# Kernel optimization log

Hardware: AMD Instinct MI355X
Metric: run time of the kernel (lower is better)

The kernel has to match this reference:

```python
import jax, jax.numpy as jnp
import numpy as np

NUM_USERS = 100000
NUM_ITEMS = 50000
EMB_DIM = 64
N_LAYERS = 3
NUM_BICLIQUES = 20000
E_ADJ = 1200000
E_HV = 400000
E_HU = 400000


def setup_inputs() -> dict:
    key = jax.random.key(0)
    ks = jax.random.split(key, 11)
    N = NUM_USERS + NUM_ITEMS
    return {
        "user_emb": jax.random.normal(ks[0], (NUM_USERS, EMB_DIM), dtype=jnp.float32) * 0.1,
        "item_emb": jax.random.normal(ks[1], (NUM_ITEMS, EMB_DIM), dtype=jnp.float32) * 0.1,
        "adj_val": jax.random.uniform(ks[2], (E_ADJ,), dtype=jnp.float32),
        "hv_val": jax.random.uniform(ks[3], (E_HV,), dtype=jnp.float32),
        "hu_val": jax.random.uniform(ks[4], (E_HU,), dtype=jnp.float32),
        "adj_row": jax.random.randint(ks[5], (E_ADJ,), 0, N, dtype=jnp.int32),
        "adj_col": jax.random.randint(ks[6], (E_ADJ,), 0, N, dtype=jnp.int32),
        "hv_row": jax.random.randint(ks[7], (E_HV,), 0, NUM_BICLIQUES, dtype=jnp.int32),
        "hv_col": jax.random.randint(ks[8], (E_HV,), 0, NUM_ITEMS, dtype=jnp.int32),
        "hu_row": jax.random.randint(ks[9], (E_HU,), 0, NUM_USERS, dtype=jnp.int32),
        "hu_col": jax.random.randint(ks[10], (E_HU,), 0, NUM_BICLIQUES, dtype=jnp.int32),
    }


def _spmm(row, col, val, x, n_rows):
    # sparse [n_rows, n_cols] @ dense [n_cols, d] via gather + segment-sum
    return jax.ops.segment_sum(val[:, None] * x[col], row, num_segments=n_rows)


def _row_degree(row, val, n_rows):
    deg = jax.ops.segment_sum(val, row, num_segments=n_rows)
    return jnp.where(deg == 0, 1.0, deg)  # matches degree[degree == 0] = 1.0


def reference(user_emb, item_emb, adj_val, hv_val, hu_val,
              adj_row, adj_col, hv_row, hv_col, hu_row, hu_col):
    N = user_emb.shape[0] + item_emb.shape[0]
    # ---- LightGCN global encoder: mean over layer embeddings ----
    all_emb = jnp.concatenate([user_emb, item_emb], axis=0)  # [N, d]
    acc = all_emb
    e = all_emb
    for _ in range(N_LAYERS):
        e = _spmm(adj_row, adj_col, adj_val, e, N)
        acc = acc + e
    final = acc / (N_LAYERS + 1)
    u_global = final[: user_emb.shape[0]]
    i_global = final[user_emb.shape[0]:]
    # ---- Biclique local encoder ----
    biclique_feat = _spmm(hv_row, hv_col, hv_val, item_emb, NUM_BICLIQUES)  # [B, d]
    biclique_feat = biclique_feat / _row_degree(hv_row, hv_val, NUM_BICLIQUES)[:, None]
    u_local = _spmm(hu_row, hu_col, hu_val, biclique_feat, user_emb.shape[0])  # [U, d]
    u_local = u_local / _row_degree(hu_row, hu_val, user_emb.shape[0])[:, None]
    return (u_global + u_local, i_global)
```

## Files before the change

kernel.cpp:

```cpp
#include <hip/hip_runtime.h>

#define NUSERS 100000
#define NITEMS 50000
#define NTOT   150000
#define NBIC   20000
#define DIM    64

#define HV_BASE  NTOT
#define HU_BASE  (NTOT + NBIC)
#define NROWS_ALL (NTOT + NBIC + NUSERS)

#define ADJ_RPB  500
#define NB_ADJ   300
#define HV_RPB   200
#define NB_HV    100
#define HU_RPB   1000
#define NB_HU    100
#define NBKT     (NB_ADJ + NB_HV + NB_HU)
#define HSIZE    512

#define EDGE_CAP 5120
#define ROWS_CAP 1024
#define CHUNK    8192
#define PA_BLK   1024
#define PB_BLK   512

typedef _Float16 h8 __attribute__((ext_vector_type(8)));

__device__ __forceinline__ void bucket_of(int r, int& b, int& rl) {
    if (r < NTOT)          { int q = r / ADJ_RPB;               b = q;                rl = r - q * ADJ_RPB; }
    else if (r < HU_BASE)  { int rr = r - HV_BASE; int q = rr / HV_RPB;
                             b = NB_ADJ + q;                    rl = rr - q * HV_RPB; }
    else                   { int rr = r - HU_BASE; int q = rr / HU_RPB;
                             b = NB_ADJ + NB_HV + q;            rl = rr - q * HU_RPB; }
}

__global__ void __launch_bounds__(PA_BLK)
phaseA_kernel(const int* __restrict__ adj_row, const int* __restrict__ adj_col,
              const float* __restrict__ adj_val,
              const int* __restrict__ hv_row, const int* __restrict__ hv_col,
              const float* __restrict__ hv_val,
              const int* __restrict__ hu_row, const int* __restrict__ hu_col,
              const float* __restrict__ hu_val,
              const float* __restrict__ user, const float* __restrict__ item,
              _Float16* __restrict__ x16,
              int* __restrict__ bkt_cnt, int2* __restrict__ tmp,
              int e_adj, int e_hv, int e_hu) {
    __shared__ int hist[HSIZE];
    __shared__ int lstart[HSIZE];
    __shared__ int destB[HSIZE];
    __shared__ int psum[HSIZE];
    __shared__ int2 stage[CHUNK];

    const int tid = threadIdx.x;
    const int e_all = e_adj + e_hv + e_hu;
    const int base = blockIdx.x * CHUNK;
    const int nloc = min(CHUNK, e_all - base);

    if (tid < HSIZE) hist[tid] = 0;
    __syncthreads();

    for (int i = tid; i < nloc; i += PA_BLK) {
        int t = base + i, r;
        if (t < e_adj)             r = adj_row[t];
        else if (t < e_adj + e_hv) r = HV_BASE + hv_row[t - e_adj];
        else                       r = HU_BASE + hu_row[t - e_adj - e_hv];
        int b, rl; bucket_of(r, b, rl);
        atomicAdd(&hist[b], 1);
    }
    __syncthreads();

    int v = 0;
    if (tid < HSIZE) { v = hist[tid]; psum[tid] = v; }
    __syncthreads();
    for (int off = 1; off < HSIZE; off <<= 1) {
        int t = 0;
        if (tid < HSIZE && tid >= off) t = psum[tid - off];
        __syncthreads();
        if (tid < HSIZE) psum[tid] += t;
        __syncthreads();
    }
    if (tid < HSIZE) lstart[tid] = psum[tid] - v;
    __syncthreads();

    if (tid < NBKT) {
        int c = hist[tid];
        if (c > 0)
            destB[tid] = tid * EDGE_CAP + atomicAdd(&bkt_cnt[tid], c) - lstart[tid];
    }
    __syncthreads();
    if (tid < HSIZE) hist[tid] = lstart[tid];
    __syncthreads();

    for (int i = tid; i < nloc; i += PA_BLK) {
        int t = base + i, r, c; float v2;
        if (t < e_adj)             { r = adj_row[t]; c = adj_col[t]; v2 = adj_val[t]; }
        else if (t < e_adj + e_hv) { int k = t - e_adj;
                                     r = HV_BASE + hv_row[k]; c = hv_col[k]; v2 = hv_val[k]; }
        else                       { int k = t - e_adj - e_hv;
                                     r = HU_BASE + hu_row[k]; c = hu_col[k]; v2 = hu_val[k]; }
        int b, rl; bucket_of(r, b, rl);
        int p = atomicAdd(&hist[b], 1);
        stage[p] = make_int2(c | (rl << 18), __float_as_int(v2));
    }
    __syncthreads();

    const int wave = tid >> 6, lane = tid & 63;
    for (int b = wave; b < NBKT; b += (PA_BLK / 64)) {
        int s = lstart[b];
        int e = hist[b];
        int d = destB[b];
        for (int j = s + lane; j < e; j += 64)
            tmp[d + j] = stage[j];
    }

    const int n8 = NTOT * DIM / 8;
    const int u8 = NUSERS * DIM / 8;
    const int gsz = gridDim.x * PA_BLK;
    for (int i = blockIdx.x * PA_BLK + tid; i < n8; i += gsz) {
        const float4* src = (i < u8) ? (const float4*)user + 2 * (size_t)i
                                     : (const float4*)item + 2 * (size_t)(i - u8);
        float4 a = src[0], b = src[1];
        h8 h;
        h[0] = (_Float16)a.x; h[1] = (_Float16)a.y; h[2] = (_Float16)a.z; h[3] = (_Float16)a.w;
        h[4] = (_Float16)b.x; h[5] = (_Float16)b.y; h[6] = (_Float16)b.z; h[7] = (_Float16)b.w;
        ((h8*)x16)[i] = h;
    }
}

__global__ void __launch_bounds__(PB_BLK)
phaseB_kernel(const int* __restrict__ bkt_cnt,
              const int2* __restrict__ tmp, int2* __restrict__ edges,
              int* __restrict__ start, int* __restrict__ cntArr) {
    __shared__ int  rh[ROWS_CAP];
    __shared__ int  rs[ROWS_CAP];
    __shared__ int  psum[PB_BLK];
    __shared__ int2 stage[EDGE_CAP];

    const int tid = threadIdx.x;
    const int b = blockIdx.x;
    int rlo, nR;
    if (b < NB_ADJ)              { rlo = b * ADJ_RPB;                          nR = ADJ_RPB; }
    else if (b < NB_ADJ + NB_HV) { rlo = HV_BASE + (b - NB_ADJ) * HV_RPB;      nR = HV_RPB; }
    else                         { rlo = HU_BASE + (b - NB_ADJ - NB_HV) * HU_RPB; nR = HU_RPB; }

    const int nE = bkt_cnt[b];

    int bv = (tid < NBKT) ? bkt_cnt[tid] : 0;
    psum[tid] = bv;
    __syncthreads();
    for (int off = 1; off < PB_BLK; off <<= 1) {
        int t = (tid >= off) ? psum[tid - off] : 0;
        __syncthreads();
        psum[tid] += t;
        __syncthreads();
    }
    const int gbase = psum[b] - nE;

    const int2* src = tmp + (size_t)b * EDGE_CAP;

    rh[tid] = 0;
    rh[tid + PB_BLK] = 0;
    __syncthreads();

    for (int i = tid; i < nE; i += PB_BLK) {
        int2 e = src[i];
        atomicAdd(&rh[((unsigned)e.x) >> 18], 1);
    }
    __syncthreads();

    int a0 = rh[2 * tid], a1 = rh[2 * tid + 1];
    int tot = a0 + a1;
    psum[tid] = tot;
    __syncthreads();
    for (int off = 1; off < PB_BLK; off <<= 1) {
        int v = (tid >= off) ? psum[tid - off] : 0;
        __syncthreads();
        psum[tid] += v;
        __syncthreads();
    }
    int ex = psum[tid] - tot;
    rs[2 * tid]     = ex;
    rs[2 * tid + 1] = ex + a0;
    __syncthreads();

    for (int i = tid; i < nR; i += PB_BLK) {
        start[rlo + i]  = gbase + rs[i];
        cntArr[rlo + i] = rh[i];
    }
    __syncthreads();

    for (int i = tid; i < nE; i += PB_BLK) {
        int2 e = src[i];
        int rl = ((unsigned)e.x) >> 18;
        int p = atomicAdd(&rs[rl], 1);
        stage[p] = make_int2(e.x & 0x3FFFF, e.y);
    }
    __syncthreads();
    for (int i = tid; i < nE; i += PB_BLK) edges[gbase + i] = stage[i];
}

__device__ __forceinline__ float gather_row(const int2* __restrict__ edges,
                                            const _Float16* __restrict__ x,
                                            int s, int n, int c, float* acc) {
    float acc1[8] = {0.f, 0.f, 0.f, 0.f, 0.f, 0.f, 0.f, 0.f};
    float ds = 0.f;
    int j = s, e = s + n;
    for (; j + 3 < e; j += 4) {
        int2 e0 = edges[j], e1 = edges[j + 1], e2 = edges[j + 2], e3 = edges[j + 3];
        float v0 = __int_as_float(e0.y), v1 = __int_as_float(e1.y);
        float v2 = __int_as_float(e2.y), v3 = __int_as_float(e3.y);
        h8 x0 = *(const h8*)(x + (size_t)e0.x * DIM + c);
        h8 x1 = *(const h8*)(x + (size_t)e1.x * DIM + c);
        h8 x2 = *(const h8*)(x + (size_t)e2.x * DIM + c);
        h8 x3 = *(const h8*)(x + (size_t)e3.x * DIM + c);
        ds += (v0 + v1) + (v2 + v3);
        #pragma unroll
        for (int k = 0; k < 8; ++k) {
            acc[k]  += v0 * (float)x0[k] + v2 * (float)x2[k];
            acc1[k] += v1 * (float)x1[k] + v3 * (float)x3[k];
        }
    }
    for (; j < e; ++j) {
        int2 e0 = edges[j];
        float v0 = __int_as_float(e0.y);
        h8 x0 = *(const h8*)(x + (size_t)e0.x * DIM + c);
        ds += v0;
        #pragma unroll
        for (int k = 0; k < 8; ++k) acc[k] += v0 * (float)x0[k];
    }
    #pragma unroll
    for (int k = 0; k < 8; ++k) acc[k] += acc1[k];
    return ds;
}

__global__ void gatherK1(const int* __restrict__ start, const int* __restrict__ cnt,
                         const int2* __restrict__ edges,
                         const _Float16* __restrict__ X16,
                         _Float16* __restrict__ T0, _Float16* __restrict__ bic,
                         int gA) {
    int c = (threadIdx.x & 7) << 3;
    int lrow = threadIdx.x >> 3;
    if (blockIdx.x < gA) {
        int r = blockIdx.x * 32 + lrow;
        if (r >= NTOT) return;
        float acc[8] = {0.f, 0.f, 0.f, 0.f, 0.f, 0.f, 0.f, 0.f};
        gather_row(edges, X16, start[r], cnt[r], c, acc);
        h8 o;
        #pragma unroll
        for (int k = 0; k < 8; ++k) o[k] = (_Float16)acc[k];
        *(h8*)(T0 + (size_t)r * DIM + c) = o;
    } else {
        int g = (blockIdx.x - gA) * 32 + lrow;
        if (g >= NBIC) return;
        int r = HV_BASE + g;
        float acc[8] = {0.f, 0.f, 0.f, 0.f, 0.f, 0.f, 0.f, 0.f};
        float deg = gather_row(edges, X16 + (size_t)NUSERS * DIM, start[r], cnt[r], c, acc);
        if (deg == 0.f) deg = 1.f;
        float inv = 1.f / deg;
        h8 o;
        #pragma unroll
        for (int k = 0; k < 8; ++k) o[k] = (_Float16)(acc[k] * inv);
        *(h8*)(bic + (size_t)g * DIM + c) = o;
    }
}

__global__ void gatherK2(const int* __restrict__ start, const int* __restrict__ cnt,
                         const int2* __restrict__ edges,
                         const _Float16* __restrict__ T0, const _Float16* __restrict__ bic,
                         _Float16* __restrict__ T1, _Float16* __restrict__ ulocal,
                         int gA) {
    int c = (threadIdx.x & 7) << 3;
    int lrow = threadIdx.x >> 3;
    if (blockIdx.x < gA) {
        int r = blockIdx.x * 32 + lrow;
        if (r >= NTOT) return;
        float acc[8] = {0.f, 0.f, 0.f, 0.f, 0.f, 0.f, 0.f, 0.f};
        gather_row(edges, T0, start[r], cnt[r], c, acc);
        h8 o;
        #pragma unroll
        for (int k = 0; k < 8; ++k) o[k] = (_Float16)acc[k];
        *(h8*)(T1 + (size_t)r * DIM + c) = o;
    } else {
        int g = (blockIdx.x - gA) * 32 + lrow;
        if (g >= NUSERS) return;
        int r = HU_BASE + g;
        float acc[8] = {0.f, 0.f, 0.f, 0.f, 0.f, 0.f, 0.f, 0.f};
        float deg = gather_row(edges, bic, start[r], cnt[r], c, acc);
        if (deg == 0.f) deg = 1.f;
        float inv = 1.f / deg;
        h8 o;
        #pragma unroll
        for (int k = 0; k < 8; ++k) o[k] = (_Float16)(acc[k] * inv);
        *(h8*)(ulocal + (size_t)g * DIM + c) = o;
    }
}

__global__ void gatherK3(const int* __restrict__ start, const int* __restrict__ cnt,
                         const int2* __restrict__ edges,
                         const _Float16* __restrict__ X16,
                         const _Float16* __restrict__ T0,
                         const _Float16* __restrict__ T1,
                         const _Float16* __restrict__ ulocal,
                         float* __restrict__ out) {
    int r = blockIdx.x * 32 + (threadIdx.x >> 3);
    if (r >= NTOT) return;
    int c = (threadIdx.x & 7) << 3;
    float acc[8] = {0.f, 0.f, 0.f, 0.f, 0.f, 0.f, 0.f, 0.f};
    gather_row(edges, T1, start[r], cnt[r], c, acc);
    size_t o = (size_t)r * DIM + c;
    h8 x0 = *(const h8*)(X16 + o);
    h8 t0 = *(const h8*)(T0 + o);
    h8 t1 = *(const h8*)(T1 + o);
    float rr[8];
    #pragma unroll
    for (int k = 0; k < 8; ++k)
        rr[k] = 0.25f * ((float)x0[k] + (float)t0[k] + (float)t1[k] + acc[k]);
    if (r < NUSERS) {
        h8 ul = *(const h8*)(ulocal + o);
        #pragma unroll
        for (int k = 0; k < 8; ++k) rr[k] += (float)ul[k];
    }
    float4 lo = make_float4(rr[0], rr[1], rr[2], rr[3]);
    float4 hi = make_float4(rr[4], rr[5], rr[6], rr[7]);
    float4* op = (float4*)(out + o);
    op[0] = lo;
    op[1] = hi;
}

extern "C" void kernel_launch(void* const* d_in, const int* in_sizes, int n_in,
                              void* d_out, int out_size, void* d_ws, size_t ws_size,
                              hipStream_t stream) {
    const float* user_emb = (const float*)d_in[0];
    const float* item_emb = (const float*)d_in[1];
    const float* adj_val  = (const float*)d_in[2];
    const float* hv_val   = (const float*)d_in[3];
    const float* hu_val   = (const float*)d_in[4];
    const int*   adj_row  = (const int*)d_in[5];
    const int*   adj_col  = (const int*)d_in[6];
    const int*   hv_row   = (const int*)d_in[7];
    const int*   hv_col   = (const int*)d_in[8];
    const int*   hu_row   = (const int*)d_in[9];
    const int*   hu_col   = (const int*)d_in[10];

    const int E_ADJ = in_sizes[2];
    const int E_HV  = in_sizes[3];
    const int E_HU  = in_sizes[4];
    const int E_ALL = E_ADJ + E_HV + E_HU;

    char* ws = (char*)d_ws;
    auto alloc = [&](size_t bytes) -> char* {
        char* p = ws;
        ws += (bytes + 255) & ~(size_t)255;
        return p;
    };
    const size_t SZ_H = (size_t)NTOT * DIM * sizeof(_Float16);
    _Float16* X16     = (_Float16*)alloc(SZ_H);
    _Float16* T0      = (_Float16*)alloc(SZ_H);
    _Float16* T1      = (_Float16*)alloc(SZ_H);
    _Float16* bic     = (_Float16*)alloc((size_t)NBIC * DIM * sizeof(_Float16));
    _Float16* ulocal  = (_Float16*)alloc((size_t)NUSERS * DIM * sizeof(_Float16));
    int*   cnt      = (int*)alloc((size_t)NROWS_ALL * sizeof(int));
    int*   start    = (int*)alloc((size_t)NROWS_ALL * sizeof(int));
    int2*  edges    = (int2*)alloc((size_t)E_ALL * sizeof(int2));
    int2*  tmp      = (int2*)alloc((size_t)NBKT * EDGE_CAP * sizeof(int2));
    int*   bkt_cnt  = (int*)alloc(NBKT * sizeof(int));

    const int BLK = 256;
    auto cdiv = [](int a, int b) { return (a + b - 1) / b; };

    hipMemsetAsync(bkt_cnt, 0, NBKT * sizeof(int), stream);
    phaseA_kernel<<<cdiv(E_ALL, CHUNK), PA_BLK, 0, stream>>>(adj_row, adj_col, adj_val,
                                                             hv_row, hv_col, hv_val,
                                                             hu_row, hu_col, hu_val,
                                                             user_emb, item_emb, X16,
                                                             bkt_cnt, tmp, E_ADJ, E_HV, E_HU);
    phaseB_kernel<<<NBKT, PB_BLK, 0, stream>>>(bkt_cnt, tmp, edges, start, cnt);

    const int gA  = cdiv(NTOT, 32);
    const int gHV = cdiv(NBIC, 32);
    const int gHU = cdiv(NUSERS, 32);

    gatherK1<<<gA + gHV, BLK, 0, stream>>>(start, cnt, edges, X16, T0, bic, gA);
    gatherK2<<<gA + gHU, BLK, 0, stream>>>(start, cnt, edges, T0, bic, T1, ulocal, gA);
    gatherK3<<<gA, BLK, 0, stream>>>(start, cnt, edges, X16, T0, T1, ulocal,
                                     (float*)d_out);
}
```

Baseline: 253.7 us.

## Sort rows by degree within 64-row windows to balance gather wavefronts

Adds a kernel that uses a wave-level bitonic sort to order each 64-row window by edge count and writes a permutation for adjacency, HV and HU rows. The three gather kernels then read row ids through this permutation, so rows of similar degree share a wavefront and lanes idle less on divergent loop lengths. The cost is an extra kernel launch, an extra indirection load per row, and scattered output writes within each window.

```diff
diff --git a/kernel.cpp b/kernel.cpp
--- a/kernel.cpp
+++ b/kernel.cpp
@@ -24,6 +24,13 @@
 #define CHUNK    8192
 #define PA_BLK   1024
 #define PB_BLK   512
+
+#define NWIN_A   ((NTOT  + 63) / 64)
+#define NWIN_HV  ((NBIC  + 63) / 64)
+#define NWIN_HU  ((NUSERS+ 63) / 64)
+#define PA_SZ    (NWIN_A  * 64)
+#define PHV_SZ   (NWIN_HV * 64)
+#define PHU_SZ   (NWIN_HU * 64)
 
 typedef _Float16 h8 __attribute__((ext_vector_type(8)));
 
@@ -200,6 +207,50 @@
     for (int i = tid; i < nE; i += PB_BLK) edges[gbase + i] = stage[i];
 }
 
+__device__ __forceinline__ void bitonic64(int& key, int& idx) {
+    const int lane = threadIdx.x & 63;
+    #pragma unroll
+    for (int k = 2; k <= 64; k <<= 1) {
+        #pragma unroll
+        for (int j = k >> 1; j > 0; j >>= 1) {
+            int pk = __shfl_xor(key, j, 64);
+            int pi = __shfl_xor(idx, j, 64);
+            bool lower = (lane & j) == 0;
+            bool asc   = (lane & k) == 0;
+            bool keepMin = (lower == asc);
+            bool greater = (key > pk) || (key == pk && idx > pi);
+            bool take = keepMin ? greater : !greater;
+            if (take) { key = pk; idx = pi; }
+        }
+    }
+}
+
+#define WPB 256
+__global__ void __launch_bounds__(WPB)
+winperm_kernel(const int* __restrict__ cnt,
+               int* __restrict__ permA, int* __restrict__ permHV,
+               int* __restrict__ permHU) {
+    const int wave = blockIdx.x * (WPB / 64) + (threadIdx.x >> 6);
+    const int lane = threadIdx.x & 63;
+    int key, idx, base;
+    int* dst;
+    if (wave < NWIN_A) {
+        base = wave * 64; idx = base + lane;
+        key = (idx < NTOT) ? cnt[idx] : 0x7fffffff;
+        dst = permA;
+    } else if (wave < NWIN_A + NWIN_HV) {
+        base = (wave - NWIN_A) * 64; idx = base + lane;
+        key = (idx < NBIC) ? cnt[HV_BASE + idx] : 0x7fffffff;
+        dst = permHV;
+    } else if (wave < NWIN_A + NWIN_HV + NWIN_HU) {
+        base = (wave - NWIN_A - NWIN_HV) * 64; idx = base + lane;
+        key = (idx < NUSERS) ? cnt[HU_BASE + idx] : 0x7fffffff;
+        dst = permHU;
+    } else return;
+    bitonic64(key, idx);
+    dst[base + lane] = idx;
+}
+
 __device__ __forceinline__ float gather_row(const int2* __restrict__ edges,
                                             const _Float16* __restrict__ x,
                                             int s, int n, int c, float* acc) {
@@ -236,13 +287,14 @@
 
 __global__ void gatherK1(const int* __restrict__ start, const int* __restrict__ cnt,
                          const int2* __restrict__ edges,
+                         const int* __restrict__ permA, const int* __restrict__ permHV,
                          const _Float16* __restrict__ X16,
                          _Float16* __restrict__ T0, _Float16* __restrict__ bic,
                          int gA) {
     int c = (threadIdx.x & 7) << 3;
     int lrow = threadIdx.x >> 3;
     if (blockIdx.x < gA) {
-        int r = blockIdx.x * 32 + lrow;
+        int r = permA[blockIdx.x * 32 + lrow];
         if (r >= NTOT) return;
         float acc[8] = {0.f, 0.f, 0.f, 0.f, 0.f, 0.f, 0.f, 0.f};
         gather_row(edges, X16, start[r], cnt[r], c, acc);
@@ -251,7 +303,7 @@
         for (int k = 0; k < 8; ++k) o[k] = (_Float16)acc[k];
         *(h8*)(T0 + (size_t)r * DIM + c) = o;
     } else {
-        int g = (blockIdx.x - gA) * 32 + lrow;
+        int g = permHV[(blockIdx.x - gA) * 32 + lrow];
         if (g >= NBIC) return;
         int r = HV_BASE + g;
         float acc[8] = {0.f, 0.f, 0.f, 0.f, 0.f, 0.f, 0.f, 0.f};
@@ -267,13 +319,14 @@
 
 __global__ void gatherK2(const int* __restrict__ start, const int* __restrict__ cnt,
                          const int2* __restrict__ edges,
+                         const int* __restrict__ permA, const int* __restrict__ permHU,
                          const _Float16* __restrict__ T0, const _Float16* __restrict__ bic,
                          _Float16* __restrict__ T1, _Float16* __restrict__ ulocal,
                          int gA) {
     int c = (threadIdx.x & 7) << 3;
     int lrow = threadIdx.x >> 3;
     if (blockIdx.x < gA) {
-        int r = blockIdx.x * 32 + lrow;
+        int r = permA[blockIdx.x * 32 + lrow];
         if (r >= NTOT) return;
         float acc[8] = {0.f, 0.f, 0.f, 0.f, 0.f, 0.f, 0.f, 0.f};
         gather_row(edges, T0, start[r], cnt[r], c, acc);
@@ -282,7 +335,7 @@
         for (int k = 0; k < 8; ++k) o[k] = (_Float16)acc[k];
         *(h8*)(T1 + (size_t)r * DIM + c) = o;
     } else {
-        int g = (blockIdx.x - gA) * 32 + lrow;
+        int g = permHU[(blockIdx.x - gA) * 32 + lrow];
         if (g >= NUSERS) return;
         int r = HU_BASE + g;
         float acc[8] = {0.f, 0.f, 0.f, 0.f, 0.f, 0.f, 0.f, 0.f};
@@ -298,12 +351,13 @@
 
 __global__ void gatherK3(const int* __restrict__ start, const int* __restrict__ cnt,
                          const int2* __restrict__ edges,
+                         const int* __restrict__ permA,
                          const _Float16* __restrict__ X16,
                          const _Float16* __restrict__ T0,
                          const _Float16* __restrict__ T1,
                          const _Float16* __restrict__ ulocal,
                          float* __restrict__ out) {
-    int r = blockIdx.x * 32 + (threadIdx.x >> 3);
+    int r = permA[blockIdx.x * 32 + (threadIdx.x >> 3)];
     if (r >= NTOT) return;
     int c = (threadIdx.x & 7) << 3;
     float acc[8] = {0.f, 0.f, 0.f, 0.f, 0.f, 0.f, 0.f, 0.f};
@@ -362,6 +416,9 @@
     _Float16* ulocal  = (_Float16*)alloc((size_t)NUSERS * DIM * sizeof(_Float16));
     int*   cnt      = (int*)alloc((size_t)NROWS_ALL * sizeof(int));
     int*   start    = (int*)alloc((size_t)NROWS_ALL * sizeof(int));
+    int*   permA    = (int*)alloc((size_t)PA_SZ  * sizeof(int));
+    int*   permHV   = (int*)alloc((size_t)PHV_SZ * sizeof(int));
+    int*   permHU   = (int*)alloc((size_t)PHU_SZ * sizeof(int));
     int2*  edges    = (int2*)alloc((size_t)E_ALL * sizeof(int2));
     int2*  tmp      = (int2*)alloc((size_t)NBKT * EDGE_CAP * sizeof(int2));
     int*   bkt_cnt  = (int*)alloc(NBKT * sizeof(int));
@@ -377,12 +434,17 @@
                                                              bkt_cnt, tmp, E_ADJ, E_HV, E_HU);
     phaseB_kernel<<<NBKT, PB_BLK, 0, stream>>>(bkt_cnt, tmp, edges, start, cnt);
 
-    const int gA  = cdiv(NTOT, 32);
-    const int gHV = cdiv(NBIC, 32);
-    const int gHU = cdiv(NUSERS, 32);
-
-    gatherK1<<<gA + gHV, BLK, 0, stream>>>(start, cnt, edges, X16, T0, bic, gA);
-    gatherK2<<<gA + gHU, BLK, 0, stream>>>(start, cnt, edges, T0, bic, T1, ulocal, gA);
-    gatherK3<<<gA, BLK, 0, stream>>>(start, cnt, edges, X16, T0, T1, ulocal,
+    const int NWAVES = NWIN_A + NWIN_HV + NWIN_HU;
+    winperm_kernel<<<cdiv(NWAVES * 64, WPB), WPB, 0, stream>>>(cnt, permA, permHV, permHU);
+
+    const int gA  = PA_SZ  / 32;
+    const int gHV = PHV_SZ / 32;
+    const int gHU = PHU_SZ / 32;
+
+    gatherK1<<<gA + gHV, BLK, 0, stream>>>(start, cnt, edges, permA, permHV,
+                                           X16, T0, bic, gA);
+    gatherK2<<<gA + gHU, BLK, 0, stream>>>(start, cnt, edges, permA, permHU,
+                                           T0, bic, T1, ulocal, gA);
+    gatherK3<<<gA, BLK, 0, stream>>>(start, cnt, edges, permA, X16, T0, T1, ulocal,
                                      (float*)d_out);
 }
```

New measurement: 268.7 us. +5.9%, slower.
